# Kernel tuning notes

Measured on AMD Instinct MI355X. Metric: run time of the kernel, lower is better.

Reference implementation:

```python
import jax, jax.numpy as jnp
import numpy as np

B, S, H, L = 64, 512, 768, 2
OP, C, M, E, A = 18, 24, 16, 8, 3
K = C + M + E          # 48 operand classes
PAD = 0                # label_pad_id


def _linear(x, W, b):
    return x @ W.T + b


def _ln(x, g, b):
    mu = x.mean(-1, keepdims=True)
    v = ((x - mu) ** 2).mean(-1, keepdims=True)
    return (x - mu) / jnp.sqrt(v + 1e-5) * g + b


def _proj(x, W, b, g, be):
    return _ln(_linear(x, W, b), g, be)


def _mlp(x, W1, b1, W2, b2):
    return _linear(jax.nn.relu(_linear(x, W1, b1)), W2, b2)


def _gru(x, hx, Wih, Whh, bih, bhh):
    # single time-step multi-layer GRU (torch nn.GRU gate math), x:[B,H], hx:[L,B,H]
    hs = []
    for l in range(L):
        gi = _linear(x, Wih[l], bih[l])
        gh = _linear(hx[l], Whh[l], bhh[l])
        ir, iz, inn = jnp.split(gi, 3, axis=-1)
        hr, hz, hn = jnp.split(gh, 3, axis=-1)
        r = jax.nn.sigmoid(ir + hr)
        z = jax.nn.sigmoid(iz + hz)
        n = jnp.tanh(inn + r * hn)
        x = (1.0 - z) * n + z * hx[l]
        hs.append(x)
    return x, jnp.stack(hs)


def _pick(idx, pc, pn, prev, bidx):
    # get_operand_vector: const -> projected const, number -> projected number, else previous result
    is_c = idx < C
    i2 = idx - C
    is_n = (i2 >= 0) & (i2 < M)
    i3 = i2 - M
    is_p = (i3 >= 0) & (i3 < E)
    v = jnp.where(is_c[:, None], pc[jnp.clip(idx, 0, C - 1)], 0.0)
    v = jnp.where(is_n[:, None], pn[bidx, jnp.clip(i2, 0, M - 1)], v)
    v = jnp.where(is_p[:, None], prev[bidx, jnp.clip(i3, 0, E - 1)], v)
    return v


def _forward(inp, const_vector, operator_vector, opj_W, opj_b, opj_g, opj_be, odj_W, odj_b, odj_g, odj_be, opc_W1, opc_b1, opc_W2, opc_b2, odc_W1, odc_b1, odc_W2, odc_b2, og_Wih, og_Whh, og_bih, og_bhh, cg_Wih, cg_Whh, cg_bih, cg_bhh, number_mask, gold_operators, gold_operands):
    Bv, Sv, Hv = inp.shape
    # _get_num_vec (concat=True): first/last token embedding per number id
    match = number_mask[:, :, None] == (jnp.arange(M) + 1)[None, None, :]   # [B,S,M]
    exists = match.any(axis=1)                                              # [B,M]
    first = jnp.argmax(match, axis=1)
    last = Sv - 1 - jnp.argmax(match[:, ::-1, :], axis=1)
    fv = jnp.take_along_axis(inp, first[..., None], axis=1)                 # [B,M,H]
    lv = jnp.take_along_axis(inp, last[..., None], axis=1)
    num_vec = jnp.where(exists[..., None], jnp.concatenate([fv, lv], -1), 0.0)  # [B,M,2H]
    pn = _proj(num_vec, odj_W, odj_b, odj_g, odj_be)                        # [B,M,H]
    pc = _proj(const_vector, odj_W, odj_b, odj_g, odj_be)                   # [C,H]
    gold_opv = _proj(operator_vector[gold_operators], opj_W, opj_b, opj_g, opj_be)  # [B,E,H]

    prev = jnp.zeros((Bv, E, Hv), inp.dtype)   # previous_result_vector
    bidx = jnp.arange(Bv)
    cv = inp[:, 0, :]
    ctx_hx = None
    op_logits, od_logits = [], []
    for i in range(E):
        if i > 0:
            cv, _ = _gru(cv, ctx_hx, cg_Wih, cg_Whh, cg_bih, cg_bhh)
        op_logits.append(_mlp(cv, opc_W1, opc_b1, opc_W2, opc_b2))
        hx = jnp.broadcast_to(cv, (L, Bv, Hv))
        step_logits = []
        pred = None
        for j in range(A):
            if j == 0:
                x = gold_opv[:, i]  # teacher forcing (module default training=True)
            else:
                x = _pick(gold_operands[:, i, j - 1], pc, pn, prev, bidx)
            x, hx = _gru(x, hx, og_Wih, og_Whh, og_bih, og_bhh)
            logit = _mlp(x, odc_W1, odc_b1, odc_W2, odc_b2)
            step_logits.append(logit)
            oidx = jnp.argmax(logit, axis=1)
            empty = jnp.max(prev[:, i, :], axis=-1) == 0
            cond = (oidx < C) & (oidx == PAD) & empty
            prev = prev.at[:, i].set(jnp.where(cond[:, None], x, prev[:, i]))
            pred = _pick(oidx, pc, pn, prev, bidx)
        empty = jnp.max(prev[:, i, :], axis=-1) == 0
        prev = prev.at[:, i].set(jnp.where(empty[:, None], pred, prev[:, i]))
        ctx_hx = jnp.broadcast_to(prev[:, i], (L, Bv, Hv))
        od_logits.append(jnp.stack(step_logits, axis=1))
    return jnp.stack(op_logits, axis=1), jnp.stack(od_logits, axis=1)


def setup_inputs() -> dict:
    key = jax.random.key(0)
    ks = iter(jax.random.split(key, 48))
    def rn(shape, s=0.02):
        return jax.random.normal(next(ks), shape, jnp.float32) * s
    d = {}
    d["input"] = jax.random.normal(next(ks), (B, S, H), jnp.float32)
    d["attention_mask"] = jax.random.randint(next(ks), (B, S), 0, 2, jnp.int32)
    d["question_mask"] = jax.random.randint(next(ks), (B, S), 0, 2, jnp.int32)
    d["number_mask"] = jax.random.randint(next(ks), (B, S), 0, M + 1, jnp.int32)
    d["gold_operators"] = jax.random.randint(next(ks), (B, E), 0, OP, jnp.int32)
    d["gold_operands"] = jax.random.randint(next(ks), (B, E, A), 0, K, jnp.int32)
    d["const_vector"] = rn((C, 2 * H), 1.0)
    d["operator_vector"] = rn((OP, 2 * H), 1.0)
    d["opj_W"] = rn((H, 2 * H)); d["opj_b"] = jnp.zeros(H); d["opj_g"] = jnp.ones(H); d["opj_be"] = jnp.zeros(H)
    d["odj_W"] = rn((H, 2 * H)); d["odj_b"] = jnp.zeros(H); d["odj_g"] = jnp.ones(H); d["odj_be"] = jnp.zeros(H)
    d["opc_W1"] = rn((H // 2, H)); d["opc_b1"] = jnp.zeros(H // 2)
    d["opc_W2"] = rn((OP, H // 2)); d["opc_b2"] = jnp.zeros(OP)
    d["odc_W1"] = rn((K // 2, H)); d["odc_b1"] = jnp.zeros(K // 2)
    d["odc_W2"] = rn((K, K // 2)); d["odc_b2"] = jnp.zeros(K)
    for p in ["og", "cg"]:
        d[p + "_Wih"] = rn((L, 3 * H, H)); d[p + "_Whh"] = rn((L, 3 * H, H))
        d[p + "_bih"] = jnp.zeros((L, 3 * H)); d[p + "_bhh"] = jnp.zeros((L, 3 * H))
    return d


def reference(input, attention_mask, question_mask, number_mask, gold_operators, gold_operands, const_vector, operator_vector, opj_W, opj_b, opj_g, opj_be, odj_W, odj_b, odj_g, odj_be, opc_W1, opc_b1, opc_W2, opc_b2, odc_W1, odc_b1, odc_W2, odc_b2, og_Wih, og_Whh, og_bih, og_bhh, cg_Wih, cg_Whh, cg_bih, cg_bhh):
    # attention_mask / question_mask are unused by the original forward as well
    return _forward(input, const_vector, operator_vector, opj_W, opj_b, opj_g, opj_be, odj_W, odj_b, odj_g, odj_be, opc_W1, opc_b1, opc_W2, opc_b2, odc_W1, odc_b1, odc_W2, odc_b2, og_Wih, og_Whh, og_bih, og_bhh, cg_Wih, cg_Whh, cg_bih, cg_bhh, number_mask, gold_operators, gold_operands)
```

## Files before the change

kernel.cpp:

```cpp
#include <hip/hip_runtime.h>
#include <math.h>

constexpr int B_  = 64;
constexpr int S_  = 512;
constexpr int H_  = 768;
constexpr int H2_ = 1536;
constexpr int G3_ = 2304;
constexpr int OP_ = 18;
constexpr int C_  = 24;
constexpr int M_  = 16;
constexpr int E_  = 8;
constexpr int A_  = 3;
constexpr int K_  = 48;
constexpr int HH_ = 384;

using f32x4  = __attribute__((ext_vector_type(4))) float;
using short8 = __attribute__((ext_vector_type(8))) short;

#define MFMA16(a, b, c) __builtin_amdgcn_mfma_f32_16x16x32_bf16((a), (b), (c), 0, 0, 0)

__device__ __forceinline__ void split1(float x, short& h, short& l)
{
    union { float f; unsigned u; } a; a.f = x;
    h = (short)(a.u >> 16);
    union { unsigned u; float f; } hb; hb.u = a.u & 0xffff0000u;
    union { float f; unsigned u; } r; r.f = x - hb.f;
    l = (short)(r.u >> 16);
}

__device__ __forceinline__ void cvt8(float4 p0, float4 p1, short8& hi, short8& lo)
{
    float x[8] = {p0.x, p0.y, p0.z, p0.w, p1.x, p1.y, p1.z, p1.w};
    #pragma unroll
    for (int e = 0; e < 8; ++e) { short h, l; split1(x[e], h, l); hi[e] = h; lo[e] = l; }
}

__global__ void k_split_all(
    const float* __restrict__ s0, short* __restrict__ h0, short* __restrict__ l0, int e0,
    const float* __restrict__ s1, short* __restrict__ h1, short* __restrict__ l1, int e1,
    const float* __restrict__ s2, short* __restrict__ h2, short* __restrict__ l2, int e2,
    const float* __restrict__ s3, short* __restrict__ h3, short* __restrict__ l3, int e3,
    const float* __restrict__ s4, short* __restrict__ h4, short* __restrict__ l4, int e4,
    const float* __restrict__ s5, short* __restrict__ h5, short* __restrict__ l5, int e5)
{
    int t = blockIdx.x * 256 + threadIdx.x;
    if (t >= e5) return;
    const float* src; short* hi; short* lo; int base;
    if      (t < e0) { src = s0; hi = h0; lo = l0; base = 0;  }
    else if (t < e1) { src = s1; hi = h1; lo = l1; base = e0; }
    else if (t < e2) { src = s2; hi = h2; lo = l2; base = e1; }
    else if (t < e3) { src = s3; hi = h3; lo = l3; base = e2; }
    else if (t < e4) { src = s4; hi = h4; lo = l4; base = e3; }
    else             { src = s5; hi = h5; lo = l5; base = e4; }
    int u = t - base;
    float4 v = ((const float4*)src)[u];
    float x[4] = {v.x, v.y, v.z, v.w};
    short h[4], l[4];
    #pragma unroll
    for (int e = 0; e < 4; ++e) split1(x[e], h[e], l[e]);
    ((short4*)hi)[u] = make_short4(h[0], h[1], h[2], h[3]);
    ((short4*)lo)[u] = make_short4(l[0], l[1], l[2], l[3]);
}

__global__ __launch_bounds__(512) void k_gru_mfma(
    const short* __restrict__ xhi, const short* __restrict__ xlo, long ldx, int pickmode,
    const int* __restrict__ gopd, int i, int jm1,
    const short* __restrict__ pchi, const short* __restrict__ pclo,
    const short* __restrict__ pnhi, const short* __restrict__ pnlo,
    const short* __restrict__ pvhi, const short* __restrict__ pvlo,
    const short* __restrict__ hhi, const short* __restrict__ hlo, long ldh,
    const short* __restrict__ Wih_hi, const short* __restrict__ Wih_lo,
    const short* __restrict__ Whh_hi, const short* __restrict__ Whh_lo,
    float* __restrict__ C)
{
    const int tid  = threadIdx.x;
    const int lane = tid & 63;
    const int w    = tid >> 6;
    const int bx   = blockIdx.x;
    const bool hside = bx >= 72;
    const int n0 = (hside ? bx - 72 : bx) * 32;
    const int koff = (lane >> 4) * 8;

    const short* ahi[4]; const short* alo[4];
    #pragma unroll
    for (int rt = 0; rt < 4; ++rt) {
        int r = rt * 16 + (lane & 15);
        long off;
        const short *bh_, *bl_;
        if (hside) { bh_ = hhi; bl_ = hlo; off = (long)r * ldh; }
        else if (!pickmode) { bh_ = xhi; bl_ = xlo; off = (long)r * ldx; }
        else {
            int idx = gopd[(r * E_ + i) * A_ + jm1];
            if (idx < C_)           { bh_ = pchi; bl_ = pclo; off = (long)idx * H_; }
            else if (idx < C_ + M_) { bh_ = pnhi; bl_ = pnlo; off = ((long)r * M_ + (idx - C_)) * H_; }
            else                    { bh_ = pvhi; bl_ = pvlo; off = ((long)r * E_ + (idx - C_ - M_)) * H_; }
        }
        ahi[rt] = bh_ + off + koff;
        alo[rt] = bl_ + off + koff;
    }
    const short* whi[2]; const short* wlo[2];
    const short* WH = hside ? Whh_hi : Wih_hi;
    const short* WL = hside ? Whh_lo : Wih_lo;
    #pragma unroll
    for (int nt = 0; nt < 2; ++nt) {
        long off = (long)(n0 + nt * 16 + (lane & 15)) * H_ + koff;
        whi[nt] = WH + off;
        wlo[nt] = WL + off;
    }

    f32x4 acc[4][2];
    #pragma unroll
    for (int rt = 0; rt < 4; ++rt)
        #pragma unroll
        for (int nt = 0; nt < 2; ++nt) acc[rt][nt] = (f32x4){0.f, 0.f, 0.f, 0.f};

    for (int kt = w * 3; kt < w * 3 + 3; ++kt) {
        const int kb = kt * 32;
        short8 Ah[4], Al[4];
        #pragma unroll
        for (int rt = 0; rt < 4; ++rt) {
            Ah[rt] = *(const short8*)(ahi[rt] + kb);
            Al[rt] = *(const short8*)(alo[rt] + kb);
        }
        #pragma unroll
        for (int nt = 0; nt < 2; ++nt) {
            short8 Bh = *(const short8*)(whi[nt] + kb);
            short8 Bl = *(const short8*)(wlo[nt] + kb);
            #pragma unroll
            for (int rt = 0; rt < 4; ++rt) {
                acc[rt][nt] = MFMA16(Ah[rt], Bh, acc[rt][nt]);
                acc[rt][nt] = MFMA16(Ah[rt], Bl, acc[rt][nt]);
                acc[rt][nt] = MFMA16(Al[rt], Bh, acc[rt][nt]);
            }
        }
    }

    __shared__ f32x4 Lr[56][64];
    if (w > 0) {
        #pragma unroll
        for (int rt = 0; rt < 4; ++rt)
            #pragma unroll
            for (int nt = 0; nt < 2; ++nt)
                Lr[(w - 1) * 8 + rt * 2 + nt][lane] = acc[rt][nt];
    }
    __syncthreads();
    if (w == 0) {
        float* Cb = C + (hside ? 2304 : 0) + n0;
        #pragma unroll
        for (int rt = 0; rt < 4; ++rt)
            #pragma unroll
            for (int nt = 0; nt < 2; ++nt) {
                int f = rt * 2 + nt;
                f32x4 s = acc[rt][nt];
                #pragma unroll
                for (int q = 0; q < 7; ++q) s = s + Lr[q * 8 + f][lane];
                int col = nt * 16 + (lane & 15);
                int rb  = rt * 16 + ((lane >> 4) << 2);
                #pragma unroll
                for (int r = 0; r < 4; ++r)
                    Cb[(long)(rb + r) * 4608 + col] = s[r];
            }
    }
}

__global__ __launch_bounds__(512) void k_proj_mfma(
    const float* __restrict__ Ab, long lda, const int* __restrict__ gidx, int Mm,
    const short* __restrict__ Whi, const short* __restrict__ Wlo, int wld,
    float* __restrict__ C, int ldc)
{
    const int tid  = threadIdx.x;
    const int lane = tid & 63;
    const int w    = tid >> 6;
    const int n0 = blockIdx.x * 64;
    const int r0 = blockIdx.y * 64;
    const int koff = (lane >> 4) * 8;

    const float* arow[4];
    #pragma unroll
    for (int rt = 0; rt < 4; ++rt) {
        int r = r0 + rt * 16 + (lane & 15);
        int rr = r < Mm ? r : (Mm - 1);
        const float* s = gidx ? (Ab + (long)gidx[rr] * lda) : (Ab + (long)rr * lda);
        arow[rt] = s + koff;
    }
    const short* whi[4]; const short* wlo[4];
    #pragma unroll
    for (int nt = 0; nt < 4; ++nt) {
        long off = (long)(n0 + nt * 16 + (lane & 15)) * wld + koff;
        whi[nt] = Whi + off; wlo[nt] = Wlo + off;
    }

    f32x4 acc[4][4];
    #pragma unroll
    for (int rt = 0; rt < 4; ++rt)
        #pragma unroll
        for (int nt = 0; nt < 4; ++nt) acc[rt][nt] = (f32x4){0.f, 0.f, 0.f, 0.f};

    for (int kt = w * 6; kt < w * 6 + 6; ++kt) {
        const int kb = kt * 32;
        short8 ah[4], al[4];
        #pragma unroll
        for (int rt = 0; rt < 4; ++rt) {
            float4 p0 = *(const float4*)(arow[rt] + kb);
            float4 p1 = *(const float4*)(arow[rt] + kb + 4);
            cvt8(p0, p1, ah[rt], al[rt]);
        }
        #pragma unroll
        for (int nt = 0; nt < 4; ++nt) {
            short8 Bh = *(const short8*)(whi[nt] + kb);
            short8 Bl = *(const short8*)(wlo[nt] + kb);
            #pragma unroll
            for (int rt = 0; rt < 4; ++rt) {
                acc[rt][nt] = MFMA16(ah[rt], Bh, acc[rt][nt]);
                acc[rt][nt] = MFMA16(ah[rt], Bl, acc[rt][nt]);
                acc[rt][nt] = MFMA16(al[rt], Bh, acc[rt][nt]);
            }
        }
    }

    __shared__ f32x4 Lr[112][64];
    if (w > 0) {
        #pragma unroll
        for (int rt = 0; rt < 4; ++rt)
            #pragma unroll
            for (int nt = 0; nt < 4; ++nt)
                Lr[(w - 1) * 16 + rt * 4 + nt][lane] = acc[rt][nt];
    }
    __syncthreads();
    if (w == 0) {
        #pragma unroll
        for (int rt = 0; rt < 4; ++rt)
            #pragma unroll
            for (int nt = 0; nt < 4; ++nt) {
                int f = rt * 4 + nt;
                f32x4 s = acc[rt][nt];
                #pragma unroll
                for (int q = 0; q < 7; ++q) s = s + Lr[q * 16 + f][lane];
                int col = n0 + nt * 16 + (lane & 15);
                int rb  = r0 + rt * 16 + ((lane >> 4) << 2);
                #pragma unroll
                for (int r = 0; r < 4; ++r)
                    if (rb + r < Mm) C[(long)(rb + r) * ldc + col] = s[r];
            }
    }
}

__global__ void k_gates2(const float* __restrict__ GI,
                         const float* __restrict__ h, long ldh,
                         const float* __restrict__ bih, const float* __restrict__ bhh,
                         float* __restrict__ hnew,
                         short* __restrict__ hnhi, short* __restrict__ hnlo)
{
    int t = blockIdx.x * 256 + threadIdx.x;
    int b = t / 768, c = t - b * 768;
    const float* gb = GI + (long)b * 4608;
    float ir  = gb[c]        + bih[c];
    float iz  = gb[768 + c]  + bih[768 + c];
    float in_ = gb[1536 + c] + bih[1536 + c];
    float hr  = gb[2304 + c] + bhh[c];
    float hz  = gb[3072 + c] + bhh[768 + c];
    float hn  = gb[3840 + c] + bhh[1536 + c];
    float r  = 1.f / (1.f + expf(-(ir + hr)));
    float z_ = 1.f / (1.f + expf(-(iz + hz)));
    float n  = tanhf(in_ + r * hn);
    float hp = h[(long)b * ldh + c];
    float v = (1.f - z_) * n + z_ * hp;
    hnew[t] = v;
    short sh, sl; split1(v, sh, sl);
    hnhi[t] = sh; hnlo[t] = sl;
}

__global__ void k_ln2(float* __restrict__ X, const float* __restrict__ bias,
                      const float* __restrict__ g, const float* __restrict__ be,
                      short* __restrict__ Xhi, short* __restrict__ Xlo)
{
    int row = blockIdx.x, tid = threadIdx.x;
    __shared__ float red[256];
    float* xr = X + (long)row * 768;
    float v[3];
    #pragma unroll
    for (int it = 0; it < 3; ++it) {
        int c2 = tid + it * 256;
        v[it] = xr[c2] + bias[c2];
    }
    float s = v[0] + v[1] + v[2];
    red[tid] = s; __syncthreads();
    for (int o = 128; o > 0; o >>= 1) { if (tid < o) red[tid] += red[tid + o]; __syncthreads(); }
    float mu = red[0] / 768.f;
    __syncthreads();
    float vv = 0.f;
    #pragma unroll
    for (int it = 0; it < 3; ++it) { float d = v[it] - mu; vv += d * d; }
    red[tid] = vv; __syncthreads();
    for (int o = 128; o > 0; o >>= 1) { if (tid < o) red[tid] += red[tid + o]; __syncthreads(); }
    float inv = 1.f / sqrtf(red[0] / 768.f + 1e-5f);
    #pragma unroll
    for (int it = 0; it < 3; ++it) {
        int c2 = tid + it * 256;
        float o2 = (v[it] - mu) * inv * g[c2] + be[c2];
        xr[c2] = o2;
        short sh, sl; split1(o2, sh, sl);
        Xhi[(long)row * 768 + c2] = sh;
        Xlo[(long)row * 768 + c2] = sl;
    }
}

__global__ __launch_bounds__(256) void k_ophead_fused(
    int do_gates,
    const float* __restrict__ GI,
    const float* __restrict__ bihg, const float* __restrict__ bhhg,
    const float* __restrict__ hp, long ldhp,
    float* __restrict__ cvf, short* __restrict__ cvhi, short* __restrict__ cvlo,
    const float* __restrict__ W1, const float* __restrict__ b1,
    const float* __restrict__ W2, const float* __restrict__ b2,
    float* __restrict__ op_out, int i)
{
    int b = blockIdx.x, tid = threadIdx.x;
    __shared__ float xs[768];
    __shared__ float hs[384];

    if (do_gates) {
        const float* gb = GI + (long)b * 4608;
        #pragma unroll
        for (int it = 0; it < 3; ++it) {
            int c2 = tid + it * 256;
            float ir  = gb[c2]        + bihg[c2];
            float iz  = gb[768 + c2]  + bihg[768 + c2];
            float in_ = gb[1536 + c2] + bihg[1536 + c2];
            float hr  = gb[2304 + c2] + bhhg[c2];
            float hz  = gb[3072 + c2] + bhhg[768 + c2];
            float hn  = gb[3840 + c2] + bhhg[1536 + c2];
            float r  = 1.f / (1.f + expf(-(ir + hr)));
            float z_ = 1.f / (1.f + expf(-(iz + hz)));
            float n  = tanhf(in_ + r * hn);
            float hpv = hp[(long)b * ldhp + c2];
            float v = (1.f - z_) * n + z_ * hpv;
            xs[c2] = v;
            cvf[(long)b * 768 + c2] = v;
            short sh, sl; split1(v, sh, sl);
            cvhi[(long)b * 768 + c2] = sh;
            cvlo[(long)b * 768 + c2] = sl;
        }
    } else {
        const float* xr = cvf + (long)b * 768;
        #pragma unroll
        for (int it = 0; it < 3; ++it) xs[tid + it * 256] = xr[tid + it * 256];
    }
    __syncthreads();

    for (int c = tid; c < 384; c += 256) {
        const float* wr = W1 + (long)c * 768;
        float acc = 0.f;
        #pragma unroll 8
        for (int k = 0; k < 768; k += 4) {
            float4 xv = *(const float4*)&xs[k];
            float4 wv = *(const float4*)(wr + k);
            acc += xv.x * wv.x + xv.y * wv.y + xv.z * wv.z + xv.w * wv.w;
        }
        hs[c] = fmaxf(acc + b1[c], 0.f);
    }
    __syncthreads();

    int c = tid >> 3, g = tid & 7;
    float acc = 0.f;
    if (c < OP_) {
        const float* wr = W2 + (long)c * HH_;
        #pragma unroll
        for (int t = 0; t < 12; ++t) {
            int k = (g + 8 * t) * 4;
            float4 xv = *(const float4*)&hs[k];
            float4 wv = *(const float4*)(wr + k);
            acc += xv.x * wv.x + xv.y * wv.y + xv.z * wv.z + xv.w * wv.w;
        }
    }
    acc += __shfl_xor(acc, 1);
    acc += __shfl_xor(acc, 2);
    acc += __shfl_xor(acc, 4);
    if (c < OP_ && g == 0)
        op_out[((long)b * E_ + i) * OP_ + c] = acc + b2[c];
}

__global__ __launch_bounds__(256) void k_odhead(
    const float* __restrict__ GI,
    const float* __restrict__ bihg, const float* __restrict__ bhhg,
    const float* __restrict__ hp, long ldhp,
    float* __restrict__ hx1f, short* __restrict__ hx1hi, short* __restrict__ hx1lo,
    const float* __restrict__ W1, const float* __restrict__ b1,
    const float* __restrict__ W2, const float* __restrict__ b2,
    float* __restrict__ od_base, long ldl,
    float* __restrict__ prev, int i,
    const float* __restrict__ pcb, const float* __restrict__ pnb,
    short* __restrict__ pvhi, short* __restrict__ pvlo,
    int do_final)
{
    int b = blockIdx.x, tid = threadIdx.x;
    __shared__ float xs[768];
    __shared__ float ps[768];
    __shared__ float hidL[24];
    __shared__ float lg[48];
    __shared__ float red[256];
    __shared__ int s_oidx;

    {
        const float* gb = GI + (long)b * 4608;
        #pragma unroll
        for (int it = 0; it < 3; ++it) {
            int c2 = tid + it * 256;
            float ir  = gb[c2]        + bihg[c2];
            float iz  = gb[768 + c2]  + bihg[768 + c2];
            float in_ = gb[1536 + c2] + bihg[1536 + c2];
            float hr  = gb[2304 + c2] + bhhg[c2];
            float hz  = gb[3072 + c2] + bhhg[768 + c2];
            float hn  = gb[3840 + c2] + bhhg[1536 + c2];
            float r  = 1.f / (1.f + expf(-(ir + hr)));
            float z_ = 1.f / (1.f + expf(-(iz + hz)));
            float n  = tanhf(in_ + r * hn);
            float hpv = hp[(long)b * ldhp + c2];
            float v = (1.f - z_) * n + z_ * hpv;
            xs[c2] = v;
            hx1f[(long)b * 768 + c2] = v;
            short sh, sl; split1(v, sh, sl);
            hx1hi[(long)b * 768 + c2] = sh;
            hx1lo[(long)b * 768 + c2] = sl;
        }
    }
    __syncthreads();

    int c = tid >> 3, g = tid & 7;
    float acc = 0.f;
    if (c < 24) {
        const float* wr = W1 + (long)c * 768;
        #pragma unroll
        for (int t = 0; t < 24; ++t) {
            int k = (g + 8 * t) * 4;
            float4 xv = *(const float4*)&xs[k];
            float4 wv = *(const float4*)(wr + k);
            acc += xv.x * wv.x + xv.y * wv.y + xv.z * wv.z + xv.w * wv.w;
        }
    }
    acc += __shfl_xor(acc, 1);
    acc += __shfl_xor(acc, 2);
    acc += __shfl_xor(acc, 4);
    if (c < 24 && g == 0) hidL[c] = fmaxf(acc + b1[c], 0.f);
    __syncthreads();

    if (tid < 48) {
        float a2 = b2[tid];
        const float* w2 = W2 + tid * 24;
        #pragma unroll
        for (int k = 0; k < 24; ++k) a2 += hidL[k] * w2[k];
        lg[tid] = a2;
        od_base[(long)b * ldl + tid] = a2;
    }

    long poff = ((long)b * E_ + i) * 768;
    float* prow = prev + poff;
    float m = -3.4e38f;
    #pragma unroll
    for (int it = 0; it < 3; ++it) m = fmaxf(m, prow[tid + it * 256]);
    red[tid] = m; __syncthreads();
    for (int o = 128; o > 0; o >>= 1) { if (tid < o) red[tid] = fmaxf(red[tid], red[tid + o]); __syncthreads(); }
    float m0 = red[0];

    if (tid == 0) {
        float best = lg[0]; int bi = 0;
        for (int k2 = 1; k2 < K_; ++k2) { float v = lg[k2]; if (v > best) { best = v; bi = k2; } }
        s_oidx = bi;
    }
    __syncthreads();
    int oidx = s_oidx;
    bool empty0 = (m0 == 0.0f);
    bool cond = (oidx == 0) && empty0;
    if (cond) {
        #pragma unroll
        for (int it = 0; it < 3; ++it) {
            int c2 = tid + it * 256;
            float v = xs[c2];
            prow[c2] = v;
            short sh, sl; split1(v, sh, sl);
            pvhi[poff + c2] = sh; pvlo[poff + c2] = sl;
        }
    }
    __syncthreads();

    if (!do_final) return;

    float mfin;
    if (cond) {
        float mx = -3.4e38f;
        #pragma unroll
        for (int it = 0; it < 3; ++it) mx = fmaxf(mx, xs[tid + it * 256]);
        red[tid] = mx; __syncthreads();
        for (int o = 128; o > 0; o >>= 1) { if (tid < o) red[tid] = fmaxf(red[tid], red[tid + o]); __syncthreads(); }
        mfin = red[0];
    } else {
        mfin = m0;
    }

    const float* src;
    if (oidx < C_)            src = pcb + (long)oidx * 768;
    else if (oidx < C_ + M_)  src = pnb + ((long)b * M_ + (oidx - C_)) * 768;
    else                      src = prev + ((long)b * E_ + (oidx - C_ - M_)) * 768;
    #pragma unroll
    for (int it = 0; it < 3; ++it) ps[tid + it * 256] = src[tid + it * 256];
    __syncthreads();

    if (mfin == 0.0f) {
        #pragma unroll
        for (int it = 0; it < 3; ++it) {
            int c2 = tid + it * 256;
            float v = ps[c2];
            prow[c2] = v;
            short sh, sl; split1(v, sh, sl);
            pvhi[poff + c2] = sh; pvlo[poff + c2] = sl;
        }
    }
}

__global__ void k_numvec(const float* __restrict__ inp, const int* __restrict__ nmask,
                         float* __restrict__ numvec)
{
    int b = blockIdx.x / M_, m = blockIdx.x % M_;
    int tid = threadIdx.x;
    int fmin = S_, lmax = -1;
    for (int s = tid; s < S_; s += 256) {
        if (nmask[b * S_ + s] == m + 1) {
            if (s < fmin) fmin = s;
            if (s > lmax) lmax = s;
        }
    }
    __shared__ int sf[256], sl[256];
    sf[tid] = fmin; sl[tid] = lmax; __syncthreads();
    for (int o = 128; o > 0; o >>= 1) {
        if (tid < o) {
            sf[tid] = min(sf[tid], sf[tid + o]);
            sl[tid] = max(sl[tid], sl[tid + o]);
        }
        __syncthreads();
    }
    int first = sf[0], last = sl[0];
    bool exists = (last >= 0);
    if (!exists) { first = 0; last = 0; }
    const float* fv = inp + ((long)b * S_ + first) * H_;
    const float* lv = inp + ((long)b * S_ + last) * H_;
    float* dst = numvec + ((long)b * M_ + m) * H2_;
    for (int h = tid; h < H_; h += 256) {
        dst[h]      = exists ? fv[h] : 0.f;
        dst[H_ + h] = exists ? lv[h] : 0.f;
    }
}

__global__ void k_copy_cv(const float* __restrict__ inp, float* __restrict__ cvv,
                          short* __restrict__ cvhi, short* __restrict__ cvlo)
{
    int b = blockIdx.x;
    for (int h = threadIdx.x; h < H_; h += 256) {
        float v = inp[(long)b * S_ * H_ + h];
        cvv[b * H_ + h] = v;
        short sh, sl; split1(v, sh, sl);
        cvhi[b * H_ + h] = sh; cvlo[b * H_ + h] = sl;
    }
}

extern "C" void kernel_launch(void* const* d_in, const int* in_sizes, int n_in,
                              void* d_out, int out_size, void* d_ws, size_t ws_size,
                              hipStream_t stream)
{
    const float* inp    = (const float*)d_in[0];
    const int*   nmask  = (const int*)  d_in[3];
    const int*   gops   = (const int*)  d_in[4];
    const int*   gopd   = (const int*)  d_in[5];
    const float* constv = (const float*)d_in[6];
    const float* opv    = (const float*)d_in[7];
    const float* opj_W  = (const float*)d_in[8];
    const float* opj_b  = (const float*)d_in[9];
    const float* opj_g  = (const float*)d_in[10];
    const float* opj_be = (const float*)d_in[11];
    const float* odj_W  = (const float*)d_in[12];
    const float* odj_b  = (const float*)d_in[13];
    const float* odj_g  = (const float*)d_in[14];
    const float* odj_be = (const float*)d_in[15];
    const float* opc_W1 = (const float*)d_in[16];
    const float* opc_b1 = (const float*)d_in[17];
    const float* opc_W2 = (const float*)d_in[18];
    const float* opc_b2 = (const float*)d_in[19];
    const float* odc_W1 = (const float*)d_in[20];
    const float* odc_b1 = (const float*)d_in[21];
    const float* odc_W2 = (const float*)d_in[22];
    const float* odc_b2 = (const float*)d_in[23];
    const float* og_Wih = (const float*)d_in[24];
    const float* og_Whh = (const float*)d_in[25];
    const float* og_bih = (const float*)d_in[26];
    const float* og_bhh = (const float*)d_in[27];
    const float* cg_Wih = (const float*)d_in[28];
    const float* cg_Whh = (const float*)d_in[29];
    const float* cg_bih = (const float*)d_in[30];
    const float* cg_bhh = (const float*)d_in[31];

    float* op_out = (float*)d_out;
    float* od_out = op_out + (long)B_ * E_ * OP_;

    float* ws      = (float*)d_ws;
    float* num_vec = ws; ws += (long)B_ * M_ * H2_;
    float* pn      = ws; ws += (long)B_ * M_ * H_;
    float* pcb     = ws; ws += (long)64 * H_;
    float* gopv    = ws; ws += (long)B_ * E_ * H_;
    float* prev    = ws; ws += (long)B_ * E_ * H_;
    float* gigh    = ws; ws += (long)B_ * 4608;
    float* cv      = ws; ws += (long)B_ * H_;
    float* h0      = ws; ws += (long)B_ * H_;
    float* hx0     = ws; ws += (long)B_ * H_;
    float* hx1     = ws; ws += (long)B_ * H_;

    auto alloc_s = [&](long elems) -> short* {
        short* p = (short*)ws; ws += elems / 2; return p;
    };
    const long nOG = (long)2 * G3_ * H_;
    short* og_ih_hi = alloc_s(nOG); short* og_ih_lo = alloc_s(nOG);
    short* og_hh_hi = alloc_s(nOG); short* og_hh_lo = alloc_s(nOG);
    short* cg_ih_hi = alloc_s(nOG); short* cg_ih_lo = alloc_s(nOG);
    short* cg_hh_hi = alloc_s(nOG); short* cg_hh_lo = alloc_s(nOG);
    const long nPJ = (long)H_ * H2_;
    short* odj_hi = alloc_s(nPJ); short* odj_lo = alloc_s(nPJ);
    short* opj_hi = alloc_s(nPJ); short* opj_lo = alloc_s(nPJ);
    short* pn_hi  = alloc_s((long)B_ * M_ * H_); short* pn_lo  = alloc_s((long)B_ * M_ * H_);
    short* pc_hi  = alloc_s((long)64 * H_);      short* pc_lo  = alloc_s((long)64 * H_);
    short* gv_hi  = alloc_s((long)B_ * E_ * H_); short* gv_lo  = alloc_s((long)B_ * E_ * H_);
    short* pv_hi  = alloc_s((long)B_ * E_ * H_); short* pv_lo  = alloc_s((long)B_ * E_ * H_);
    short* cv_hi  = alloc_s((long)B_ * H_);      short* cv_lo  = alloc_s((long)B_ * H_);
    short* h0_hi  = alloc_s((long)B_ * H_);      short* h0_lo  = alloc_s((long)B_ * H_);
    short* hx0_hi = alloc_s((long)B_ * H_);      short* hx0_lo = alloc_s((long)B_ * H_);
    short* hx1_hi = alloc_s((long)B_ * H_);      short* hx1_lo = alloc_s((long)B_ * H_);

    hipMemsetAsync(prev, 0, (size_t)B_ * E_ * H_ * sizeof(float), stream);
    hipMemsetAsync(pv_hi, 0, (size_t)2 * B_ * E_ * H_ * sizeof(short), stream);

    {
        int nOG4 = (int)(nOG / 4), nPJ4 = (int)(nPJ / 4);
        int e0 = nOG4, e1 = 2 * nOG4, e2 = 3 * nOG4, e3 = 4 * nOG4;
        int e4 = e3 + nPJ4, e5 = e4 + nPJ4;
        k_split_all<<<(e5 + 255) / 256, 256, 0, stream>>>(
            og_Wih, og_ih_hi, og_ih_lo, e0,
            og_Whh, og_hh_hi, og_hh_lo, e1,
            cg_Wih, cg_ih_hi, cg_ih_lo, e2,
            cg_Whh, cg_hh_hi, cg_hh_lo, e3,
            odj_W,  odj_hi,  odj_lo,  e4,
            opj_W,  opj_hi,  opj_lo,  e5);
    }

    k_numvec<<<B_ * M_, 256, 0, stream>>>(inp, nmask, num_vec);

    k_proj_mfma<<<dim3(12, 16), 512, 0, stream>>>(num_vec, H2_, nullptr, 1024,
                                                  odj_hi, odj_lo, H2_, pn, H_);
    k_ln2<<<1024, 256, 0, stream>>>(pn, odj_b, odj_g, odj_be, pn_hi, pn_lo);

    k_proj_mfma<<<dim3(12, 1), 512, 0, stream>>>(constv, H2_, nullptr, C_,
                                                 odj_hi, odj_lo, H2_, pcb, H_);
    k_ln2<<<C_, 256, 0, stream>>>(pcb, odj_b, odj_g, odj_be, pc_hi, pc_lo);

    k_proj_mfma<<<dim3(12, 8), 512, 0, stream>>>(opv, H2_, gops, 512,
                                                 opj_hi, opj_lo, H2_, gopv, H_);
    k_ln2<<<512, 256, 0, stream>>>(gopv, opj_b, opj_g, opj_be, gv_hi, gv_lo);

    k_copy_cv<<<B_, 256, 0, stream>>>(inp, cv, cv_hi, cv_lo);

    const long ldE = (long)E_ * H_;
    const long lW  = (long)G3_ * H_;

    for (int i = 0; i < E_; ++i) {
        if (i > 0) {
            const float* hrow = prev + (long)(i - 1) * H_;
            const short* hrhi = pv_hi + (long)(i - 1) * H_;
            const short* hrlo = pv_lo + (long)(i - 1) * H_;
            k_gru_mfma<<<144, 512, 0, stream>>>(cv_hi, cv_lo, H_, 0, nullptr, 0, 0,
                                                nullptr, nullptr, nullptr, nullptr, nullptr, nullptr,
                                                hrhi, hrlo, ldE,
                                                cg_ih_hi, cg_ih_lo, cg_hh_hi, cg_hh_lo, gigh);
            k_gates2<<<192, 256, 0, stream>>>(gigh, hrow, ldE, cg_bih, cg_bhh, h0, h0_hi, h0_lo);
            k_gru_mfma<<<144, 512, 0, stream>>>(h0_hi, h0_lo, H_, 0, nullptr, 0, 0,
                                                nullptr, nullptr, nullptr, nullptr, nullptr, nullptr,
                                                hrhi, hrlo, ldE,
                                                cg_ih_hi + lW, cg_ih_lo + lW,
                                                cg_hh_hi + lW, cg_hh_lo + lW, gigh);
            k_ophead_fused<<<B_, 256, 0, stream>>>(1, gigh, cg_bih + G3_, cg_bhh + G3_,
                                                   hrow, ldE, cv, cv_hi, cv_lo,
                                                   opc_W1, opc_b1, opc_W2, opc_b2, op_out, i);
        } else {
            k_ophead_fused<<<B_, 256, 0, stream>>>(0, gigh, cg_bih, cg_bhh,
                                                   cv, H_, cv, cv_hi, cv_lo,
                                                   opc_W1, opc_b1, opc_W2, opc_b2, op_out, i);
        }

        for (int j = 0; j < A_; ++j) {
            const short *xhi, *xlo; long ldx; int pickm;
            if (j == 0) { xhi = gv_hi + (long)i * H_; xlo = gv_lo + (long)i * H_; ldx = ldE; pickm = 0; }
            else        { xhi = nullptr; xlo = nullptr; ldx = 0; pickm = 1; }
            const float* hp0 = (j == 0) ? cv : hx0;
            const float* hp1 = (j == 0) ? cv : hx1;
            const short* hp0hi = (j == 0) ? cv_hi : hx0_hi;
            const short* hp0lo = (j == 0) ? cv_lo : hx0_lo;
            const short* hp1hi = (j == 0) ? cv_hi : hx1_hi;
            const short* hp1lo = (j == 0) ? cv_lo : hx1_lo;

            k_gru_mfma<<<144, 512, 0, stream>>>(xhi, xlo, ldx, pickm, gopd, i, j - 1,
                                                pc_hi, pc_lo, pn_hi, pn_lo, pv_hi, pv_lo,
                                                hp0hi, hp0lo, H_,
                                                og_ih_hi, og_ih_lo, og_hh_hi, og_hh_lo, gigh);
            k_gates2<<<192, 256, 0, stream>>>(gigh, hp0, H_, og_bih, og_bhh, hx0, hx0_hi, hx0_lo);
            k_gru_mfma<<<144, 512, 0, stream>>>(hx0_hi, hx0_lo, H_, 0, nullptr, 0, 0,
                                                nullptr, nullptr, nullptr, nullptr, nullptr, nullptr,
                                                hp1hi, hp1lo, H_,
                                                og_ih_hi + lW, og_ih_lo + lW,
                                                og_hh_hi + lW, og_hh_lo + lW, gigh);

            float* od_base = od_out + ((long)i * A_ + j) * K_;
            k_odhead<<<B_, 256, 0, stream>>>(gigh, og_bih + G3_, og_bhh + G3_,
                                             hp1, H_, hx1, hx1_hi, hx1_lo,
                                             odc_W1, odc_b1, odc_W2, odc_b2,
                                             od_base, (long)E_ * A_ * K_,
                                             prev, i, pcb, pn, pv_hi, pv_lo,
                                             (j == A_ - 1) ? 1 : 0);
        }
    }
}
```

Measured before the change: 1.403 ms.

## Precompute operator-GRU input gates for all steps in one batched GEMM

The j==0 operator-GRU input projection depends only on the projected gold-operator vectors, so all E steps are now computed up front in one batched k_gi_pre GEMM. Inside the loop, the j==0 step launches only the hidden-side half (72 blocks). k_gates2 gains separate strides for the input and hidden gate buffers. The MFMA split-K reduction is also changed so all 8 waves each reduce and store one fragment, instead of wave 0 doing all of it. The cost is an extra workspace buffer and one larger upfront GEMM.

```diff
diff --git a/kernel.cpp b/kernel.cpp
--- a/kernel.cpp
+++ b/kernel.cpp
@@ -63,6 +63,7 @@
 }
 
 __global__ __launch_bounds__(512) void k_gru_mfma(
+    int ghonly,
     const short* __restrict__ xhi, const short* __restrict__ xlo, long ldx, int pickmode,
     const int* __restrict__ gopd, int i, int jm1,
     const short* __restrict__ pchi, const short* __restrict__ pclo,
@@ -77,8 +78,8 @@
     const int lane = tid & 63;
     const int w    = tid >> 6;
     const int bx   = blockIdx.x;
-    const bool hside = bx >= 72;
-    const int n0 = (hside ? bx - 72 : bx) * 32;
+    const bool hside = ghonly || (bx >= 72);
+    const int n0 = ((hside && !ghonly) ? bx - 72 : bx) * 32;
     const int koff = (lane >> 4) * 8;
 
     const short* ahi[4]; const short* alo[4];
@@ -135,31 +136,100 @@
         }
     }
 
-    __shared__ f32x4 Lr[56][64];
-    if (w > 0) {
-        #pragma unroll
-        for (int rt = 0; rt < 4; ++rt)
+    __shared__ f32x4 Lr[8][8][64];
+    #pragma unroll
+    for (int rt = 0; rt < 4; ++rt)
+        #pragma unroll
+        for (int nt = 0; nt < 2; ++nt)
+            Lr[w][rt * 2 + nt][lane] = acc[rt][nt];
+    __syncthreads();
+    {
+        const int f  = w;
+        const int rt = f >> 1, nt = f & 1;
+        f32x4 s = Lr[0][f][lane];
+        #pragma unroll
+        for (int q = 1; q < 8; ++q) s = s + Lr[q][f][lane];
+        float* Cb = C + (hside ? 2304 : 0) + n0;
+        int col = nt * 16 + (lane & 15);
+        int rb  = rt * 16 + ((lane >> 4) << 2);
+        #pragma unroll
+        for (int r = 0; r < 4; ++r)
+            Cb[(long)(rb + r) * 4608 + col] = s[r];
+    }
+}
+
+__global__ __launch_bounds__(512) void k_gi_pre(
+    const short* __restrict__ xhi, const short* __restrict__ xlo,
+    const short* __restrict__ Whi, const short* __restrict__ Wlo,
+    float* __restrict__ C)
+{
+    const int tid  = threadIdx.x;
+    const int lane = tid & 63;
+    const int w    = tid >> 6;
+    const int n0 = blockIdx.x * 32;
+    const int r0 = blockIdx.y * 64;
+    const int koff = (lane >> 4) * 8;
+
+    const short* ahi[4]; const short* alo[4];
+    #pragma unroll
+    for (int rt = 0; rt < 4; ++rt) {
+        long off = (long)(r0 + rt * 16 + (lane & 15)) * H_ + koff;
+        ahi[rt] = xhi + off;
+        alo[rt] = xlo + off;
+    }
+    const short* whi[2]; const short* wlo[2];
+    #pragma unroll
+    for (int nt = 0; nt < 2; ++nt) {
+        long off = (long)(n0 + nt * 16 + (lane & 15)) * H_ + koff;
+        whi[nt] = Whi + off;
+        wlo[nt] = Wlo + off;
+    }
+
+    f32x4 acc[4][2];
+    #pragma unroll
+    for (int rt = 0; rt < 4; ++rt)
+        #pragma unroll
+        for (int nt = 0; nt < 2; ++nt) acc[rt][nt] = (f32x4){0.f, 0.f, 0.f, 0.f};
+
+    for (int kt = w * 3; kt < w * 3 + 3; ++kt) {
+        const int kb = kt * 32;
+        short8 Ah[4], Al[4];
+        #pragma unroll
+        for (int rt = 0; rt < 4; ++rt) {
+            Ah[rt] = *(const short8*)(ahi[rt] + kb);
+            Al[rt] = *(const short8*)(alo[rt] + kb);
+        }
+        #pragma unroll
+        for (int nt = 0; nt < 2; ++nt) {
+            short8 Bh = *(const short8*)(whi[nt] + kb);
+            short8 Bl = *(const short8*)(wlo[nt] + kb);
             #pragma unroll
-            for (int nt = 0; nt < 2; ++nt)
-                Lr[(w - 1) * 8 + rt * 2 + nt][lane] = acc[rt][nt];
-    }
-    __syncthreads();
-    if (w == 0) {
-        float* Cb = C + (hside ? 2304 : 0) + n0;
-        #pragma unroll
-        for (int rt = 0; rt < 4; ++rt)
-            #pragma unroll
-            for (int nt = 0; nt < 2; ++nt) {
-                int f = rt * 2 + nt;
-                f32x4 s = acc[rt][nt];
-                #pragma unroll
-                for (int q = 0; q < 7; ++q) s = s + Lr[q * 8 + f][lane];
-                int col = nt * 16 + (lane & 15);
-                int rb  = rt * 16 + ((lane >> 4) << 2);
-                #pragma unroll
-                for (int r = 0; r < 4; ++r)
-                    Cb[(long)(rb + r) * 4608 + col] = s[r];
+            for (int rt = 0; rt < 4; ++rt) {
+                acc[rt][nt] = MFMA16(Ah[rt], Bh, acc[rt][nt]);
+                acc[rt][nt] = MFMA16(Ah[rt], Bl, acc[rt][nt]);
+                acc[rt][nt] = MFMA16(Al[rt], Bh, acc[rt][nt]);
             }
+        }
+    }
+
+    __shared__ f32x4 Lr[8][8][64];
+    #pragma unroll
+    for (int rt = 0; rt < 4; ++rt)
+        #pragma unroll
+        for (int nt = 0; nt < 2; ++nt)
+            Lr[w][rt * 2 + nt][lane] = acc[rt][nt];
+    __syncthreads();
+    {
+        const int f  = w;
+        const int rt = f >> 1, nt = f & 1;
+        f32x4 s = Lr[0][f][lane];
+        #pragma unroll
+        for (int q = 1; q < 8; ++q) s = s + Lr[q][f][lane];
+        int col = n0 + nt * 16 + (lane & 15);
+        int rb  = r0 + rt * 16 + ((lane >> 4) << 2);
+        #pragma unroll
+        for (int r = 0; r < 4; ++r)
+            C[(long)(rb + r) * G3_ + col] = s[r];
     }
 }
 
@@ -245,7 +315,8 @@
     }
 }
 
-__global__ void k_gates2(const float* __restrict__ GI,
+__global__ void k_gates2(const float* __restrict__ GI, long ldgi,
+                         const float* __restrict__ GH, long ldgh,
                          const float* __restrict__ h, long ldh,
                          const float* __restrict__ bih, const float* __restrict__ bhh,
                          float* __restrict__ hnew,
@@ -253,13 +324,14 @@
 {
     int t = blockIdx.x * 256 + threadIdx.x;
     int b = t / 768, c = t - b * 768;
-    const float* gb = GI + (long)b * 4608;
-    float ir  = gb[c]        + bih[c];
-    float iz  = gb[768 + c]  + bih[768 + c];
-    float in_ = gb[1536 + c] + bih[1536 + c];
-    float hr  = gb[2304 + c] + bhh[c];
-    float hz  = gb[3072 + c] + bhh[768 + c];
-    float hn  = gb[3840 + c] + bhh[1536 + c];
+    const float* gi = GI + (long)b * ldgi;
+    const float* gh = GH + (long)b * ldgh;
+    float ir  = gi[c]        + bih[c];
+    float iz  = gi[768 + c]  + bih[768 + c];
+    float in_ = gi[1536 + c] + bih[1536 + c];
+    float hr  = gh[c]        + bhh[c];
+    float hz  = gh[768 + c]  + bhh[768 + c];
+    float hn  = gh[1536 + c] + bhh[1536 + c];
     float r  = 1.f / (1.f + expf(-(ir + hr)));
     float z_ = 1.f / (1.f + expf(-(iz + hz)));
     float n  = tanhf(in_ + r * hn);
@@ -607,6 +679,7 @@
     float* gopv    = ws; ws += (long)B_ * E_ * H_;
     float* prev    = ws; ws += (long)B_ * E_ * H_;
     float* gigh    = ws; ws += (long)B_ * 4608;
+    float* gi_pre  = ws; ws += (long)B_ * E_ * G3_;
     float* cv      = ws; ws += (long)B_ * H_;
     float* h0      = ws; ws += (long)B_ * H_;
     float* hx0     = ws; ws += (long)B_ * H_;
@@ -662,6 +735,8 @@
                                                  opj_hi, opj_lo, H2_, gopv, H_);
     k_ln2<<<512, 256, 0, stream>>>(gopv, opj_b, opj_g, opj_be, gv_hi, gv_lo);
 
+    k_gi_pre<<<dim3(72, 8), 512, 0, stream>>>(gv_hi, gv_lo, og_ih_hi, og_ih_lo, gi_pre);
+
     k_copy_cv<<<B_, 256, 0, stream>>>(inp, cv, cv_hi, cv_lo);
 
     const long ldE = (long)E_ * H_;
@@ -672,12 +747,13 @@
             const float* hrow = prev + (long)(i - 1) * H_;
             const short* hrhi = pv_hi + (long)(i - 1) * H_;
             const short* hrlo = pv_lo + (long)(i - 1) * H_;
-            k_gru_mfma<<<144, 512, 0, stream>>>(cv_hi, cv_lo, H_, 0, nullptr, 0, 0,
+            k_gru_mfma<<<144, 512, 0, stream>>>(0, cv_hi, cv_lo, H_, 0, nullptr, 0, 0,
                                                 nullptr, nullptr, nullptr, nullptr, nullptr, nullptr,
                                                 hrhi, hrlo, ldE,
                                                 cg_ih_hi, cg_ih_lo, cg_hh_hi, cg_hh_lo, gigh);
-            k_gates2<<<192, 256, 0, stream>>>(gigh, hrow, ldE, cg_bih, cg_bhh, h0, h0_hi, h0_lo);
-            k_gru_mfma<<<144, 512, 0, stream>>>(h0_hi, h0_lo, H_, 0, nullptr, 0, 0,
+            k_gates2<<<192, 256, 0, stream>>>(gigh, 4608, gigh + 2304, 4608,
+                                              hrow, ldE, cg_bih, cg_bhh, h0, h0_hi, h0_lo);
+            k_gru_mfma<<<144, 512, 0, stream>>>(0, h0_hi, h0_lo, H_, 0, nullptr, 0, 0,
                                                 nullptr, nullptr, nullptr, nullptr, nullptr, nullptr,
                                                 hrhi, hrlo, ldE,
                                                 cg_ih_hi + lW, cg_ih_lo + lW,
@@ -692,9 +768,6 @@
         }
 
         for (int j = 0; j < A_; ++j) {
-            const short *xhi, *xlo; long ldx; int pickm;
-            if (j == 0) { xhi = gv_hi + (long)i * H_; xlo = gv_lo + (long)i * H_; ldx = ldE; pickm = 0; }
-            else        { xhi = nullptr; xlo = nullptr; ldx = 0; pickm = 1; }
             const float* hp0 = (j == 0) ? cv : hx0;
             const float* hp1 = (j == 0) ? cv : hx1;
             const short* hp0hi = (j == 0) ? cv_hi : hx0_hi;
@@ -702,12 +775,23 @@
             const short* hp1hi = (j == 0) ? cv_hi : hx1_hi;
             const short* hp1lo = (j == 0) ? cv_lo : hx1_lo;
 
-            k_gru_mfma<<<144, 512, 0, stream>>>(xhi, xlo, ldx, pickm, gopd, i, j - 1,
-                                                pc_hi, pc_lo, pn_hi, pn_lo, pv_hi, pv_lo,
-                                                hp0hi, hp0lo, H_,
-                                                og_ih_hi, og_ih_lo, og_hh_hi, og_hh_lo, gigh);
-            k_gates2<<<192, 256, 0, stream>>>(gigh, hp0, H_, og_bih, og_bhh, hx0, hx0_hi, hx0_lo);
-            k_gru_mfma<<<144, 512, 0, stream>>>(hx0_hi, hx0_lo, H_, 0, nullptr, 0, 0,
+            if (j == 0) {
+                k_gru_mfma<<<72, 512, 0, stream>>>(1, nullptr, nullptr, 0, 0, nullptr, 0, 0,
+                                                   nullptr, nullptr, nullptr, nullptr, nullptr, nullptr,
+                                                   hp0hi, hp0lo, H_,
+                                                   og_ih_hi, og_ih_lo, og_hh_hi, og_hh_lo, gigh);
+                k_gates2<<<192, 256, 0, stream>>>(gi_pre + (long)i * G3_, (long)E_ * G3_,
+                                                  gigh + 2304, 4608,
+                                                  hp0, H_, og_bih, og_bhh, hx0, hx0_hi, hx0_lo);
+            } else {
+                k_gru_mfma<<<144, 512, 0, stream>>>(0, nullptr, nullptr, 0, 1, gopd, i, j - 1,
+                                                    pc_hi, pc_lo, pn_hi, pn_lo, pv_hi, pv_lo,
+                                                    hp0hi, hp0lo, H_,
+                                                    og_ih_hi, og_ih_lo, og_hh_hi, og_hh_lo, gigh);
+                k_gates2<<<192, 256, 0, stream>>>(gigh, 4608, gigh + 2304, 4608,
+                                                  hp0, H_, og_bih, og_bhh, hx0, hx0_hi, hx0_lo);
+            }
+            k_gru_mfma<<<144, 512, 0, stream>>>(0, hx0_hi, hx0_lo, H_, 0, nullptr, 0, 0,
                                                 nullptr, nullptr, nullptr, nullptr, nullptr, nullptr,
                                                 hp1hi, hp1lo, H_,
                                                 og_ih_hi + lW, og_ih_lo + lW,
```

Result: no change. 1.395 ms, median of 2 (-0.6%).
